# Performance work log

Hardware: AMD Instinct MI355X
Metric: run time of the kernel (lower is better)

## Reference

```python
import jax, jax.numpy as jnp
import numpy as np

B, S, C = 65536, 49, 19


def setup_inputs() -> dict:
    key = jax.random.key(0)
    k1, k2, k3, k4, k5 = jax.random.split(key, 5)
    return {
        "H_factor": jax.random.normal(k1, (B, S, C), dtype=jnp.float32),
        "H_hybrid": jax.random.normal(k2, (B, S, C), dtype=jnp.float32),
        "W_alpha": jax.random.normal(k3, (C, C), dtype=jnp.float32),
        "W_beta": jax.random.normal(k4, (C, C), dtype=jnp.float32),
        "W_out": jax.random.normal(k5, (S, C), dtype=jnp.float32),
        "bias": jnp.zeros((1,), dtype=jnp.float32),
    }


def reference(H_factor, H_hybrid, W_alpha, W_beta, W_out, bias):
    # alpha/beta: softmax-gated over last (channel) dim, shapes [B, S, C]
    alpha = jax.nn.softmax(jnp.einsum("bsc,cd->bsd", H_factor, W_alpha), axis=-1)
    beta = jax.nn.softmax(jnp.einsum("bsc,cd->bsd", H_hybrid, W_beta), axis=-1)
    H_final = alpha * H_factor + beta * H_hybrid  # [B, S, C]
    # weighted full reduction over (S, C) -> [B], plus broadcast bias [1]
    u = jnp.sum(H_final * W_out, axis=(1, 2)) + bias
    return jax.nn.sigmoid(u)
```

## Files before the change

### kernel.cpp

```cpp
#include <hip/hip_runtime.h>


#define BB    65536
#define S     49
#define C     19
#define G     4
#define SC    (S * C)
#define BLOCK 256
#define PAIRS (G * S)

__global__ __launch_bounds__(BLOCK)
void wfl_kernel(const float* __restrict__ Hf, const float* __restrict__ Hh,
                const float* __restrict__ Wa, const float* __restrict__ Wb,
                const float* __restrict__ Wo, const float* __restrict__ bias,
                float* __restrict__ out)
{
    __shared__ __align__(16) float lds_hf[G * SC];
    __shared__ __align__(16) float lds_hh[G * SC];
    __shared__ float lds_wo[SC];
    __shared__ float lds_part[PAIRS];

    const int t   = threadIdx.x;
    const int blk = blockIdx.x;
    const long base = (long)blk * (G * SC);

    const float4* gf = (const float4*)(Hf + base);
    const float4* gh = (const float4*)(Hh + base);
    float4* lf = (float4*)lds_hf;
    float4* lh = (float4*)lds_hh;
#pragma unroll
    for (int k = 0; k < 4; ++k) {
        int idx = t + k * BLOCK;
        if (idx < (G * SC) / 4) {
            lf[idx] = gf[idx];
            lh[idx] = gh[idx];
        }
    }
#pragma unroll
    for (int k = 0; k < 4; ++k) {
        int idx = t + k * BLOCK;
        if (idx < SC) lds_wo[idx] = Wo[idx];
    }
    __syncthreads();

    if (t < PAIRS) {
        const int s = t % S;
        const float* hfp = &lds_hf[t * C];
        const float* hhp = &lds_hh[t * C];
        const float* wop = &lds_wo[s * C];

        float vhf[C], vhh[C], vwo[C];
#pragma unroll
        for (int c = 0; c < C; ++c) {
            vhf[c] = hfp[c];
            vhh[c] = hhp[c];
            vwo[c] = wop[c];
        }

        float part = 0.f;

        {
            float l[C];
#pragma unroll
            for (int d = 0; d < C; ++d) l[d] = 0.f;
#pragma unroll
            for (int c = 0; c < C; ++c) {
                const float h = vhf[c];
#pragma unroll
                for (int d = 0; d < C; ++d)
                    l[d] = fmaf(h, Wa[c * C + d], l[d]);
            }
            float m = l[0];
#pragma unroll
            for (int d = 1; d < C; ++d) m = fmaxf(m, l[d]);
            float num = 0.f, den = 0.f;
#pragma unroll
            for (int d = 0; d < C; ++d) {
                const float e = __expf(l[d] - m);
                den += e;
                num = fmaf(e, vhf[d] * vwo[d], num);
            }
            part += num / den;
        }

        {
            float l[C];
#pragma unroll
            for (int d = 0; d < C; ++d) l[d] = 0.f;
#pragma unroll
            for (int c = 0; c < C; ++c) {
                const float h = vhh[c];
#pragma unroll
                for (int d = 0; d < C; ++d)
                    l[d] = fmaf(h, Wb[c * C + d], l[d]);
            }
            float m = l[0];
#pragma unroll
            for (int d = 1; d < C; ++d) m = fmaxf(m, l[d]);
            float num = 0.f, den = 0.f;
#pragma unroll
            for (int d = 0; d < C; ++d) {
                const float e = __expf(l[d] - m);
                den += e;
                num = fmaf(e, vhh[d] * vwo[d], num);
            }
            part += num / den;
        }

        lds_part[t] = part;
    }
    __syncthreads();

    if (t < G) {
        float u = bias[0];
#pragma unroll
        for (int s2 = 0; s2 < S; ++s2) u += lds_part[t * S + s2];
        out[blk * G + t] = 1.f / (1.f + __expf(-u));
    }
}

extern "C" void kernel_launch(void* const* d_in, const int* in_sizes, int n_in,
                              void* d_out, int out_size, void* d_ws, size_t ws_size,
                              hipStream_t stream)
{
    const float* Hf   = (const float*)d_in[0];
    const float* Hh   = (const float*)d_in[1];
    const float* Wa   = (const float*)d_in[2];
    const float* Wb   = (const float*)d_in[3];
    const float* Wo   = (const float*)d_in[4];
    const float* bias = (const float*)d_in[5];
    float* out = (float*)d_out;

    const int blocks = BB / G;
    wfl_kernel<<<blocks, BLOCK, 0, stream>>>(Hf, Hh, Wa, Wb, Wo, bias, out);
}
```

Measured before the change: 519.2 us.

## Map one wavefront per 64 (b,s) pairs with atomic batch reduction

```diff
diff --git a/kernel.cpp b/kernel.cpp
--- a/kernel.cpp
+++ b/kernel.cpp
@@ -4,119 +4,106 @@
 #define BB    65536
 #define S     49
 #define C     19
-#define G     4
-#define SC    (S * C)
-#define BLOCK 256
-#define PAIRS (G * S)
+#define NPAIR (BB * S)
+#define PPB   64
+#define NBLK  (NPAIR / PPB)
 
-__global__ __launch_bounds__(BLOCK)
-void wfl_kernel(const float* __restrict__ Hf, const float* __restrict__ Hh,
-                const float* __restrict__ Wa, const float* __restrict__ Wb,
-                const float* __restrict__ Wo, const float* __restrict__ bias,
-                float* __restrict__ out)
+__global__ __launch_bounds__(PPB, 8)
+void wfl_main(const float* __restrict__ Hf, const float* __restrict__ Hh,
+              const float* __restrict__ Wa, const float* __restrict__ Wb,
+              const float* __restrict__ Wo, float* __restrict__ ws)
 {
-    __shared__ __align__(16) float lds_hf[G * SC];
-    __shared__ __align__(16) float lds_hh[G * SC];
-    __shared__ float lds_wo[SC];
-    __shared__ float lds_part[PAIRS];
+    __shared__ __align__(16) float lh[PPB * C];
 
-    const int t   = threadIdx.x;
-    const int blk = blockIdx.x;
-    const long base = (long)blk * (G * SC);
+    const int lane = threadIdx.x;
+    const int blk  = blockIdx.x;
+    const int p0   = blk * PPB;
+    const int p    = p0 + lane;
+    const int b    = p / S;
+    const int s    = p - b * S;
 
-    const float4* gf = (const float4*)(Hf + base);
-    const float4* gh = (const float4*)(Hh + base);
-    float4* lf = (float4*)lds_hf;
-    float4* lh = (float4*)lds_hh;
+    const float* __restrict__ wop = Wo + s * C;
+    const float* hp = lh + lane * C;
+    float4* l4 = (float4*)lh;
+
+    float part = 0.f;
+
+    {
+        const float4* g4 = (const float4*)(Hf + (size_t)p0 * C);
 #pragma unroll
-    for (int k = 0; k < 4; ++k) {
-        int idx = t + k * BLOCK;
-        if (idx < (G * SC) / 4) {
-            lf[idx] = gf[idx];
-            lh[idx] = gh[idx];
+        for (int k = 0; k < 5; ++k) {
+            int i = lane + k * PPB;
+            if (i < (PPB * C) / 4) l4[i] = g4[i];
         }
-    }
+        __syncthreads();
+
+        float l[C];
 #pragma unroll
-    for (int k = 0; k < 4; ++k) {
-        int idx = t + k * BLOCK;
-        if (idx < SC) lds_wo[idx] = Wo[idx];
-    }
-    __syncthreads();
-
-    if (t < PAIRS) {
-        const int s = t % S;
-        const float* hfp = &lds_hf[t * C];
-        const float* hhp = &lds_hh[t * C];
-        const float* wop = &lds_wo[s * C];
-
-        float vhf[C], vhh[C], vwo[C];
+        for (int d = 0; d < C; ++d) l[d] = 0.f;
 #pragma unroll
         for (int c = 0; c < C; ++c) {
-            vhf[c] = hfp[c];
-            vhh[c] = hhp[c];
-            vwo[c] = wop[c];
+            const float h = hp[c];
+#pragma unroll
+            for (int d = 0; d < C; ++d)
+                l[d] = fmaf(h, Wa[c * C + d], l[d]);
         }
+        float den = 0.f, num = 0.f;
+#pragma unroll
+        for (int d = 0; d < C; ++d) {
+            const float e = __expf(l[d]);
+            den += e;
+            num = fmaf(e * hp[d], wop[d], num);
+        }
+        part = fmaf(num, __builtin_amdgcn_rcpf(den), part);
+        __syncthreads();
+    }
 
-        float part = 0.f;
+    {
+        const float4* g4 = (const float4*)(Hh + (size_t)p0 * C);
+#pragma unroll
+        for (int k = 0; k < 5; ++k) {
+            int i = lane + k * PPB;
+            if (i < (PPB * C) / 4) l4[i] = g4[i];
+        }
+        __syncthreads();
 
-        {
-            float l[C];
+        float l[C];
 #pragma unroll
-            for (int d = 0; d < C; ++d) l[d] = 0.f;
+        for (int d = 0; d < C; ++d) l[d] = 0.f;
 #pragma unroll
-            for (int c = 0; c < C; ++c) {
-                const float h = vhf[c];
+        for (int c = 0; c < C; ++c) {
+            const float h = hp[c];
 #pragma unroll
-                for (int d = 0; d < C; ++d)
-                    l[d] = fmaf(h, Wa[c * C + d], l[d]);
-            }
-            float m = l[0];
+            for (int d = 0; d < C; ++d)
+                l[d] = fmaf(h, Wb[c * C + d], l[d]);
+        }
+        float den = 0.f, num = 0.f;
 #pragma unroll
-            for (int d = 1; d < C; ++d) m = fmaxf(m, l[d]);
-            float num = 0.f, den = 0.f;
+        for (int d = 0; d < C; ++d) {
+            const float e = __expf(l[d]);
+            den += e;
+            num = fmaf(e * hp[d], wop[d], num);
+        }
+        part = fmaf(num, __builtin_amdgcn_rcpf(den), part);
+    }
+
+    const int b0 = p0 / S;
 #pragma unroll
-            for (int d = 0; d < C; ++d) {
-                const float e = __expf(l[d] - m);
-                den += e;
-                num = fmaf(e, vhf[d] * vwo[d], num);
-            }
-            part += num / den;
-        }
+    for (int k = 0; k < 3; ++k) {
+        float v = ((b - b0) == k) ? part : 0.f;
+#pragma unroll
+        for (int off = 32; off; off >>= 1) v += __shfl_xor(v, off, 64);
+        if (lane == 0 && (b0 + k) < BB) unsafeAtomicAdd(&ws[b0 + k], v);
+    }
+}
 
-        {
-            float l[C];
-#pragma unroll
-            for (int d = 0; d < C; ++d) l[d] = 0.f;
-#pragma unroll
-            for (int c = 0; c < C; ++c) {
-                const float h = vhh[c];
-#pragma unroll
-                for (int d = 0; d < C; ++d)
-                    l[d] = fmaf(h, Wb[c * C + d], l[d]);
-            }
-            float m = l[0];
-#pragma unroll
-            for (int d = 1; d < C; ++d) m = fmaxf(m, l[d]);
-            float num = 0.f, den = 0.f;
-#pragma unroll
-            for (int d = 0; d < C; ++d) {
-                const float e = __expf(l[d] - m);
-                den += e;
-                num = fmaf(e, vhh[d] * vwo[d], num);
-            }
-            part += num / den;
-        }
-
-        lds_part[t] = part;
-    }
-    __syncthreads();
-
-    if (t < G) {
-        float u = bias[0];
-#pragma unroll
-        for (int s2 = 0; s2 < S; ++s2) u += lds_part[t * S + s2];
-        out[blk * G + t] = 1.f / (1.f + __expf(-u));
-    }
+__global__ __launch_bounds__(256)
+void wfl_fin(const float* __restrict__ ws, const float* __restrict__ bias,
+             float* __restrict__ out)
+{
+    const int i = blockIdx.x * 256 + threadIdx.x;
+    const float u = ws[i] + bias[0];
+    out[i] = __builtin_amdgcn_rcpf(1.f + __expf(-u));
 }
 
 extern "C" void kernel_launch(void* const* d_in, const int* in_sizes, int n_in,
@@ -130,7 +117,9 @@
     const float* Wo   = (const float*)d_in[4];
     const float* bias = (const float*)d_in[5];
     float* out = (float*)d_out;
+    float* acc = (float*)d_ws;
 
-    const int blocks = BB / G;
-    wfl_kernel<<<blocks, BLOCK, 0, stream>>>(Hf, Hh, Wa, Wb, Wo, bias, out);
+    hipMemsetAsync(acc, 0, BB * sizeof(float), stream);
+    wfl_main<<<NBLK, PPB, 0, stream>>>(Hf, Hh, Wa, Wb, Wo, acc);
+    wfl_fin<<<BB / 256, 256, 0, stream>>>(acc, bias, out);
 }
```

Measured after the change: 511.2 us. Within noise of the previous version (-1.5%).
